# Kernel optimization log

Measured on AMD Instinct MI355X. Metric: run time of the kernel, lower is better.

The kernel has to match this reference:

```python
import jax, jax.numpy as jnp
import numpy as np

HIS = 10   # history steps (node_feature_dim = 10*4)
ROLL = 2   # args.pred_roll
MP = 2     # message_passing_steps
N = 20000  # num nodes (balls)
E = 320000 # num edges


def _mlp(x, W1, b1, W2, b2, g, be):
    # two-layer ELU MLP + BatchNorm1d (training mode: batch statistics)
    h = jax.nn.elu(x @ W1 + b1)
    h = jax.nn.elu(h @ W2 + b2)
    B, M, C = h.shape
    f = h.reshape(B * M, C)
    mu = f.mean(0)
    var = ((f - mu) ** 2).mean(0)  # biased variance, as torch BN training
    f = (f - mu) * jax.lax.rsqrt(var + 1e-5) * g + be
    return f.reshape(B, M, C)


def setup_inputs() -> dict:
    key = jax.random.key(0)
    ks = jax.random.split(key, 16)

    def lin(k, i, o):
        W = jax.random.normal(k, (i, o), jnp.float32) / jnp.sqrt(jnp.float32(i))
        b = jnp.full((o,), 0.1, jnp.float32)
        return W, b

    inp = {}
    inp["nodes"] = jax.random.normal(ks[0], (1, HIS + ROLL, N, 4), jnp.float32)
    inp["edge_pair"] = jax.random.randint(ks[1], (E, 2), 0, N)
    inp["edge_attr"] = jax.random.normal(ks[2], (E, 2), jnp.float32)
    # encoder node MLP: 40 -> 128 -> 128
    inp["en_W1"], inp["en_b1"] = lin(ks[3], 40, 128)
    inp["en_W2"], inp["en_b2"] = lin(ks[4], 128, 128)
    inp["en_g"], inp["en_be"] = jnp.ones((128,), jnp.float32), jnp.zeros((128,), jnp.float32)
    # encoder edge MLP: 6 -> 32 -> 32
    inp["ee_W1"], inp["ee_b1"] = lin(ks[5], 6, 32)
    inp["ee_W2"], inp["ee_b2"] = lin(ks[6], 32, 32)
    inp["ee_g"], inp["ee_be"] = jnp.ones((32,), jnp.float32), jnp.zeros((32,), jnp.float32)
    # GraphNetBlock edge MLP: 288 -> 128 -> 32
    inp["ge_W1"], inp["ge_b1"] = lin(ks[7], 288, 128)
    inp["ge_W2"], inp["ge_b2"] = lin(ks[8], 128, 32)
    inp["ge_g"], inp["ge_be"] = jnp.ones((32,), jnp.float32), jnp.zeros((32,), jnp.float32)
    # GraphNetBlock node MLP: 160 -> 256 -> 128
    inp["gn_W1"], inp["gn_b1"] = lin(ks[9], 160, 256)
    inp["gn_W2"], inp["gn_b2"] = lin(ks[10], 256, 128)
    inp["gn_g"], inp["gn_be"] = jnp.ones((128,), jnp.float32), jnp.zeros((128,), jnp.float32)
    # decoder: Linear(128,128) Tanh Linear(128,2)
    inp["d_W1"], inp["d_b1"] = lin(ks[11], 128, 128)
    inp["d_W2"], inp["d_b2"] = lin(ks[12], 128, 2)
    return inp


def _forward(nodes, edge_pair, edge_attr,
             en_W1, en_b1, en_W2, en_b2, en_g, en_be,
             ee_W1, ee_b1, ee_W2, ee_b2, ee_g, ee_be,
             ge_W1, ge_b1, ge_W2, ge_b2, ge_g, ge_be,
             gn_W1, gn_b1, gn_W2, gn_b2, gn_g, gn_be,
             d_W1, d_b1, d_W2, d_b2):
    window = nodes[0]                 # [T, N, 4]
    n = window.shape[1]
    s0 = edge_pair[:, 0]
    s1 = edge_pair[:, 1]
    # history features: [1, N, HIS*4]
    history = jnp.transpose(window[:HIS], (1, 0, 2)).reshape(1, n, -1)
    gt_future = window[HIS:]          # [ROLL, N, 4]
    # initial edge features: raw 2-dim attr + |pos/vel diff| (4-dim) -> 6
    pd0 = jnp.abs(window[HIS][s0] - window[HIS][s1])   # [E, 4]
    edge_feat = jnp.concatenate([edge_attr[None], pd0[None]], -1)  # [1, E, 6]
    cur_pos = window[HIS - 1, :, :2]
    cur_vel = window[HIS - 1, :, 2:]
    preds = []
    for _ in range(ROLL):
        ln = _mlp(history, en_W1, en_b1, en_W2, en_b2, en_g, en_be)    # [1,N,128]
        le = _mlp(edge_feat, ee_W1, ee_b1, ee_W2, ee_b2, ee_g, ee_be)  # [1,E,32]
        for _ in range(MP):
            # edge update: gather sender/receiver, MLP
            ef = jnp.concatenate([ln[:, s0], ln[:, s1], le], -1)       # [1,E,288]
            ne = _mlp(ef, ge_W1, ge_b1, ge_W2, ge_b2, ge_g, ge_be)     # [1,E,32]
            # node aggregation: scatter-add at both endpoints
            agg = jnp.zeros((n, ne.shape[-1]), ne.dtype)
            agg = agg.at[s0].add(ne[0]).at[s1].add(ne[0])
            nf = jnp.concatenate([ln, agg[None]], -1)                  # [1,N,160]
            nn_ = _mlp(nf, gn_W1, gn_b1, gn_W2, gn_b2, gn_g, gn_be)
            ln = nn_ + ln
            le = ne + le
        accel = jnp.tanh(ln @ d_W1 + d_b1) @ d_W2 + d_b2               # [1,N,2]
        prev_pos = cur_pos
        cur_pos = 2 * cur_pos + accel - prev_pos                       # [1,N,2]
        cur_vel = cur_vel + accel
        pd = jnp.abs(cur_pos[:, s0] - cur_pos[:, s1])                  # [1,E,2]
        edge_feat = edge_feat.at[:, :, -2:].set(pd)
        preds.append(cur_pos)
        hist4 = history.reshape(1, n, HIS, 4)
        new_state = jnp.concatenate([cur_pos.reshape(1, n, 1, 2),
                                     cur_vel.reshape(1, n, 1, 2)], -1)
        history = jnp.concatenate([hist4[:, :, 1:, :], new_state], -2).reshape(1, n, -1)
    preds = jnp.stack(preds, 1)                                        # [1,ROLL,N,2]
    diff = preds[0] - gt_future[:, :, :2]
    variance = 5e-5
    loss_nll = (diff ** 2 / (2 * variance)).sum() / (ROLL * n)
    loss_mse = (diff ** 2).mean()
    return preds, loss_nll, loss_mse, gt_future


def reference(nodes, edge_pair, edge_attr,
              en_W1, en_b1, en_W2, en_b2, en_g, en_be,
              ee_W1, ee_b1, ee_W2, ee_b2, ee_g, ee_be,
              ge_W1, ge_b1, ge_W2, ge_b2, ge_g, ge_be,
              gn_W1, gn_b1, gn_W2, gn_b2, gn_g, gn_be,
              d_W1, d_b1, d_W2, d_b2):
    return _forward(nodes, edge_pair, edge_attr,
                    en_W1, en_b1, en_W2, en_b2, en_g, en_be,
                    ee_W1, ee_b1, ee_W2, ee_b2, ee_g, ee_be,
                    ge_W1, ge_b1, ge_W2, ge_b2, ge_g, ge_be,
                    gn_W1, gn_b1, gn_W2, gn_b2, gn_g, gn_be,
                    d_W1, d_b1, d_W2, d_b2)
```

## Files before the change

kernel.cpp:

```cpp
#include <hip/hip_runtime.h>


constexpr int NN = 20000;
constexpr int NE = 320000;
constexpr int NSLOT = 32;
constexpr int SSTR = 512;

typedef __attribute__((ext_vector_type(8))) short short8;
typedef __attribute__((ext_vector_type(4))) float f32x4;

__device__ __forceinline__ float act_elu(float x) { return x > 0.f ? x : __expf(x) - 1.f; }
__device__ __forceinline__ unsigned short f2bf(float f) {
  unsigned u = __builtin_bit_cast(unsigned, f);
  return (unsigned short)((u + 0x7FFFu + ((u >> 16) & 1u)) >> 16);
}
__device__ __forceinline__ float bf2f(unsigned short h) {
  unsigned u = ((unsigned)h) << 16; return __builtin_bit_cast(float, u);
}

template<int K1, int K1P, int C1, int C2, int BM, int NWM, int NWC, int NWM2, int NWC2,
         int ACT2, bool STATS, int MODE>
__global__ __launch_bounds__(256) void mlp2_k(
    const unsigned short* __restrict__ A,
    const unsigned short* __restrict__ Wt1, const float* __restrict__ b1,
    const unsigned short* __restrict__ Wt2, const float* __restrict__ b2,
    unsigned short* __restrict__ out, int M, float* __restrict__ stat,
    float* __restrict__ aggF, const float* __restrict__ statP, float invE,
    const float* __restrict__ gg, const float* __restrict__ gb,
    float* __restrict__ sclW, const int* __restrict__ dg0, const int* __restrict__ dg1)
{
  constexpr int FM  = BM / (16 * NWM);
  constexpr int FC  = C1 / (16 * NWC);
  constexpr int FM2 = BM / (16 * NWM2);
  constexpr int FC2 = C2 / (16 * NWC2);
  constexpr int NKS1 = K1P / 32;
  constexpr int NKS2 = C1 / 32;
  constexpr int AST = K1P + 8;
  constexpr int P1 = C1 + 8;
  constexpr int P2 = C2 + 8;
  constexpr int ACH = K1P / 8;
  static_assert(NWM * NWC == 4 && NWM2 * NWC2 == 4, "4 waves");
  static_assert(C2 <= C1, "repack reuses H1");

  __shared__ unsigned short As[BM * AST];
  __shared__ unsigned short H1[BM * P1];
  __shared__ float red[2][C2];
  __shared__ float s_scl[(MODE == 4) ? 32 : 1], s_shf[(MODE == 4) ? 32 : 1];

  const int tid = threadIdx.x;
  const int row0 = blockIdx.x * BM;
  const int wave = tid >> 6, lane = tid & 63;
  const int wm = wave % NWM, wc = wave / NWM;
  const int wm2 = wave % NWM2, wc2 = wave / NWM2;
  const int lr = lane & 15, kg = lane >> 4;

  if (STATS) for (int i = tid; i < 2 * C2; i += 256) ((float*)red)[i] = 0.f;

  if constexpr (MODE == 4) {
    if (tid < 32) {
      float su = 0.f, sq = 0.f;
      for (int s = 0; s < NSLOT; ++s) {
        su += statP[(size_t)s * SSTR + tid];
        sq += statP[(size_t)s * SSTR + 256 + tid];
      }
      float mu = su * invE;
      float var = sq * invE - mu * mu;
      float sc = rsqrtf(var + 1e-5f) * gg[tid];
      float sh = gb[tid] - mu * sc;
      s_scl[tid] = sc; s_shf[tid] = sh;
      if (blockIdx.x == 0) { sclW[tid] = sc; sclW[32 + tid] = sh; }
    }
    __syncthreads();
  }

  for (int idx = tid; idx < BM * ACH; idx += 256) {
    int m = idx / ACH, chk = idx % ACH;
    int kglob = chk * 8;
    int row = row0 + m;
    uint4 v = make_uint4(0, 0, 0, 0);
    if (row < M) {
      if constexpr (MODE == 0) {
        if (kglob + 8 <= K1) v = *(const uint4*)(A + (size_t)row * K1 + kglob);
      } else if constexpr (MODE == 3) {
        if (chk == 0) v = *(const uint4*)(A + (size_t)row * 8);
      } else {
        if (kglob < 128) {
          v = *(const uint4*)(A + (size_t)row * 128 + kglob);
        } else {
          int c0 = kglob - 128;
          float* ap = &aggF[(size_t)row * 32 + c0];
          float4 a0 = *(float4*)ap, a1 = *(float4*)(ap + 4);
          *(float4*)ap = make_float4(0.f, 0.f, 0.f, 0.f);
          *(float4*)(ap + 4) = make_float4(0.f, 0.f, 0.f, 0.f);
          float d = (float)(dg0[row] + dg1[row]);
          float av[8] = {a0.x, a0.y, a0.z, a0.w, a1.x, a1.y, a1.z, a1.w};
          unsigned short* vp = (unsigned short*)&v;
#pragma unroll
          for (int j = 0; j < 8; ++j)
            vp[j] = f2bf(fmaf(s_scl[c0 + j], av[j], d * s_shf[c0 + j]));
        }
      }
    }
    *(uint4*)&As[m * AST + chk * 8] = v;
  }
  __syncthreads();

  f32x4 acc1[FM][FC];
#pragma unroll
  for (int i = 0; i < FM; ++i)
#pragma unroll
    for (int j = 0; j < FC; ++j) acc1[i][j] = (f32x4){0.f, 0.f, 0.f, 0.f};

#pragma unroll
  for (int ks = 0; ks < NKS1; ++ks) {
    const int k0 = ks * 32;
    short8 af[FM], bfr[FC];
#pragma unroll
    for (int i = 0; i < FM; ++i) {
      int r = (wm * FM + i) * 16 + lr;
      af[i] = __builtin_bit_cast(short8, *(const uint4*)&As[r * AST + k0 + kg * 8]);
    }
#pragma unroll
    for (int j = 0; j < FC; ++j) {
      int c = (wc * FC + j) * 16 + lr;
      bfr[j] = __builtin_bit_cast(short8, *(const uint4*)&Wt1[(size_t)c * K1P + k0 + kg * 8]);
    }
#pragma unroll
    for (int i = 0; i < FM; ++i)
#pragma unroll
      for (int j = 0; j < FC; ++j)
        acc1[i][j] = __builtin_amdgcn_mfma_f32_16x16x32_bf16(af[i], bfr[j], acc1[i][j], 0, 0, 0);
  }

  {
    float bl1[FC];
#pragma unroll
    for (int j = 0; j < FC; ++j) bl1[j] = b1[(wc * FC + j) * 16 + lr];
#pragma unroll
    for (int i = 0; i < FM; ++i)
#pragma unroll
      for (int t = 0; t < 4; ++t) {
        int rl = (wm * FM + i) * 16 + kg * 4 + t;
#pragma unroll
        for (int j = 0; j < FC; ++j)
          H1[rl * P1 + (wc * FC + j) * 16 + lr] = f2bf(act_elu(acc1[i][j][t] + bl1[j]));
      }
  }
  __syncthreads();

  f32x4 acc2[FM2][FC2];
#pragma unroll
  for (int i = 0; i < FM2; ++i)
#pragma unroll
    for (int j = 0; j < FC2; ++j) acc2[i][j] = (f32x4){0.f, 0.f, 0.f, 0.f};

#pragma unroll
  for (int ks = 0; ks < NKS2; ++ks) {
    const int k0 = ks * 32;
    short8 af[FM2], bfr[FC2];
#pragma unroll
    for (int i = 0; i < FM2; ++i) {
      int r = (wm2 * FM2 + i) * 16 + lr;
      af[i] = __builtin_bit_cast(short8, *(const uint4*)&H1[r * P1 + k0 + kg * 8]);
    }
#pragma unroll
    for (int j = 0; j < FC2; ++j) {
      int c = (wc2 * FC2 + j) * 16 + lr;
      bfr[j] = __builtin_bit_cast(short8, *(const uint4*)&Wt2[(size_t)c * C1 + k0 + kg * 8]);
    }
#pragma unroll
    for (int i = 0; i < FM2; ++i)
#pragma unroll
      for (int j = 0; j < FC2; ++j)
        acc2[i][j] = __builtin_amdgcn_mfma_f32_16x16x32_bf16(af[i], bfr[j], acc2[i][j], 0, 0, 0);
  }
  __syncthreads();

  float psum[FC2], psq[FC2], bl2[FC2];
#pragma unroll
  for (int j = 0; j < FC2; ++j) {
    psum[j] = 0.f; psq[j] = 0.f;
    bl2[j] = b2[(wc2 * FC2 + j) * 16 + lr];
  }
#pragma unroll
  for (int i = 0; i < FM2; ++i)
#pragma unroll
    for (int t = 0; t < 4; ++t) {
      int rl = (wm2 * FM2 + i) * 16 + kg * 4 + t;
      bool ok = (row0 + rl) < M;
#pragma unroll
      for (int j = 0; j < FC2; ++j) {
        float v = acc2[i][j][t] + bl2[j];
        if (ACT2 == 1) v = act_elu(v);
        else if (ACT2 == 2) v = tanhf(v);
        if (STATS && ok) { psum[j] += v; psq[j] += v * v; }
        H1[rl * P2 + (wc2 * FC2 + j) * 16 + lr] = f2bf(v);
      }
    }
  if (STATS) {
#pragma unroll
    for (int j = 0; j < FC2; ++j) {
      int c = (wc2 * FC2 + j) * 16 + lr;
      atomicAdd(&red[0][c], psum[j]);
      atomicAdd(&red[1][c], psq[j]);
    }
  }
  __syncthreads();
  for (int idx = tid; idx < BM * (C2 / 8); idx += 256) {
    int r = idx / (C2 / 8), cc = idx % (C2 / 8);
    int row = row0 + r;
    if (row < M)
      *(uint4*)&out[(size_t)row * C2 + cc * 8] = *(const uint4*)&H1[r * P2 + cc * 8];
  }
  if (STATS) {
    float* st = stat + (size_t)(blockIdx.x & (NSLOT - 1)) * SSTR;
    for (int i = tid; i < C2; i += 256) {
      atomicAdd(&st[i], red[0][i]);
      atomicAdd(&st[256 + i], red[1][i]);
    }
  }
}

template<int K, int C, int BM, int NWM, int NWC, int ACT, int DEC>
__global__ __launch_bounds__(256) void mgemm_k(
    const unsigned short* __restrict__ A,
    const unsigned short* __restrict__ Wt, const float* __restrict__ bias,
    unsigned short* __restrict__ out, int M,
    const float* __restrict__ W2f, const float* __restrict__ b2f,
    float* __restrict__ pos, float* __restrict__ vel, float* __restrict__ preds)
{
  constexpr int FM = BM / (16 * NWM);
  constexpr int FC = C / (16 * NWC);
  constexpr int NKS = K / 32;
  constexpr int AST = K + 8;
  constexpr int P2 = C + 8;
  constexpr int ACH = K / 8;
  static_assert(NWM * NWC == 4, "4 waves");

  __shared__ unsigned short As[BM * AST];
  __shared__ unsigned short Ob[BM * P2];
  __shared__ float Wl[DEC ? 256 : 1];

  const int tid = threadIdx.x;
  const int row0 = blockIdx.x * BM;
  const int wave = tid >> 6, lane = tid & 63;
  const int wm = wave % NWM, wc = wave / NWM;
  const int lr = lane & 15, kg = lane >> 4;

  for (int idx = tid; idx < BM * ACH; idx += 256) {
    int m = idx / ACH, chk = idx % ACH;
    int row = row0 + m;
    uint4 v = make_uint4(0, 0, 0, 0);
    if (row < M) v = *(const uint4*)(A + (size_t)row * K + chk * 8);
    *(uint4*)&As[m * AST + chk * 8] = v;
  }
  __syncthreads();

  f32x4 acc[FM][FC];
#pragma unroll
  for (int i = 0; i < FM; ++i)
#pragma unroll
    for (int j = 0; j < FC; ++j) acc[i][j] = (f32x4){0.f, 0.f, 0.f, 0.f};

#pragma unroll
  for (int ks = 0; ks < NKS; ++ks) {
    const int k0 = ks * 32;
    short8 af[FM], bfr[FC];
#pragma unroll
    for (int i = 0; i < FM; ++i) {
      int r = (wm * FM + i) * 16 + lr;
      af[i] = __builtin_bit_cast(short8, *(const uint4*)&As[r * AST + k0 + kg * 8]);
    }
#pragma unroll
    for (int j = 0; j < FC; ++j) {
      int c = (wc * FC + j) * 16 + lr;
      bfr[j] = __builtin_bit_cast(short8, *(const uint4*)&Wt[(size_t)c * K + k0 + kg * 8]);
    }
#pragma unroll
    for (int i = 0; i < FM; ++i)
#pragma unroll
      for (int j = 0; j < FC; ++j)
        acc[i][j] = __builtin_amdgcn_mfma_f32_16x16x32_bf16(af[i], bfr[j], acc[i][j], 0, 0, 0);
  }

  float bl[FC];
#pragma unroll
  for (int j = 0; j < FC; ++j) bl[j] = bias[(wc * FC + j) * 16 + lr];
#pragma unroll
  for (int i = 0; i < FM; ++i)
#pragma unroll
    for (int t = 0; t < 4; ++t) {
      int rl = (wm * FM + i) * 16 + kg * 4 + t;
#pragma unroll
      for (int j = 0; j < FC; ++j) {
        float v = acc[i][j][t] + bl[j];
        if (ACT == 1) v = act_elu(v);
        else if (ACT == 2) v = tanhf(v);
        Ob[rl * P2 + (wc * FC + j) * 16 + lr] = f2bf(v);
      }
    }
  if constexpr (DEC) Wl[tid] = W2f[tid];
  __syncthreads();
  if constexpr (DEC) {
    int rloc = tid >> 3, j = tid & 7;
    int row = row0 + rloc;
    float ax = 0.f, ay = 0.f;
#pragma unroll
    for (int kk = 0; kk < 16; ++kk) {
      int k = j + 8 * kk;
      float f = bf2f(Ob[rloc * P2 + k]);
      ax = fmaf(f, Wl[2 * k], ax);
      ay = fmaf(f, Wl[2 * k + 1], ay);
    }
    ax += __shfl_down(ax, 4, 8); ax += __shfl_down(ax, 2, 8); ax += __shfl_down(ax, 1, 8);
    ay += __shfl_down(ay, 4, 8); ay += __shfl_down(ay, 2, 8); ay += __shfl_down(ay, 1, 8);
    if (j == 0 && row < M) {
      float axx = ax + b2f[0], ayy = ay + b2f[1];
      float2 p = ((float2*)pos)[row], vv = ((float2*)vel)[row];
      p.x += axx; p.y += ayy; vv.x += axx; vv.y += ayy;
      ((float2*)pos)[row] = p; ((float2*)vel)[row] = vv;
      ((float2*)preds)[row] = p;
    }
  } else {
    for (int idx = tid; idx < BM * (C / 8); idx += 256) {
      int r = idx / (C / 8), cc = idx % (C / 8);
      int row = row0 + r;
      if (row < M)
        *(uint4*)&out[(size_t)row * C + cc * 8] = *(const uint4*)&Ob[r * P2 + cc * 8];
    }
  }
}

template<int WOUT, int LEFUSE>
__global__ __launch_bounds__(256) void ge_edge_k(
    const unsigned short* __restrict__ Pb,
    const unsigned short* __restrict__ leb,
    const unsigned short* __restrict__ e32prev,
    const float* __restrict__ sclshf,
    const int* __restrict__ epP,
    const unsigned short* __restrict__ Wt1c,
    const float* __restrict__ b1,
    const unsigned short* __restrict__ Wt2,
    const float* __restrict__ b2,
    unsigned short* __restrict__ out,
    float* __restrict__ aggF,
    float* __restrict__ stat)
{
  constexpr int BM = 64;
  constexpr int P1 = 136;
  __shared__ unsigned short Ps[BM * P1];
  __shared__ unsigned short As[BM * 40];
  __shared__ float red[2][32];
  __shared__ int eps[BM * 2];

  const int tid = threadIdx.x;
  const int e0 = blockIdx.x * BM;
  const int wave = tid >> 6, lane = tid & 63;
  const int lr = lane & 15, kg = lane >> 4;
  const int wm = wave & 1, wc = wave >> 1;

  uint4 g0[4], g1[4];
  int gm[4], gch[4];
#pragma unroll
  for (int t = 0; t < 4; ++t) {
    int idx = tid + 256 * t;
    int m = idx >> 4, ch = idx & 15;
    gm[t] = m; gch[t] = ch;
    int s0 = epP[2 * (e0 + m)];
    int s1 = epP[2 * (e0 + m) + 1];
    g0[t] = *(const uint4*)&Pb[(size_t)s0 * 256 + ch * 8];
    g1[t] = *(const uint4*)&Pb[(size_t)s1 * 256 + 128 + ch * 8];
  }

  if (tid < BM * 2) eps[tid] = epP[e0 * 2 + tid];
  {
    int m = tid >> 2, chk = tid & 3;
    uint4 lv = *(const uint4*)&leb[(size_t)(e0 + m) * 32 + chk * 8];
    if constexpr (LEFUSE) {
      uint4 ev = *(const uint4*)&e32prev[(size_t)(e0 + m) * 32 + chk * 8];
      const unsigned short* lp = (const unsigned short*)&lv;
      const unsigned short* epv = (const unsigned short*)&ev;
      uint4 ov;
      unsigned short* op = (unsigned short*)&ov;
#pragma unroll
      for (int j = 0; j < 8; ++j) {
        int c = chk * 8 + j;
        op[j] = f2bf(bf2f(lp[j]) + fmaf(sclshf[c], bf2f(epv[j]), sclshf[32 + c]));
      }
      *(uint4*)&As[m * 40 + chk * 8] = ov;
    } else {
      *(uint4*)&As[m * 40 + chk * 8] = lv;
    }
  }
  short8 wf1[4];
#pragma unroll
  for (int j = 0; j < 4; ++j)
    wf1[j] = __builtin_bit_cast(short8, *(const uint4*)&Wt1c[(size_t)((wc * 4 + j) * 16 + lr) * 32 + kg * 8]);
  if (tid < 64) ((float*)red)[tid] = 0.f;
  __syncthreads();

  f32x4 acc1[2][4];
#pragma unroll
  for (int i = 0; i < 2; ++i)
#pragma unroll
    for (int j = 0; j < 4; ++j) acc1[i][j] = (f32x4){0.f, 0.f, 0.f, 0.f};
  {
    short8 af[2];
#pragma unroll
    for (int i = 0; i < 2; ++i)
      af[i] = __builtin_bit_cast(short8, *(const uint4*)&As[((wm * 2 + i) * 16 + lr) * 40 + kg * 8]);
#pragma unroll
    for (int i = 0; i < 2; ++i)
#pragma unroll
      for (int j = 0; j < 4; ++j)
        acc1[i][j] = __builtin_amdgcn_mfma_f32_16x16x32_bf16(af[i], wf1[j], acc1[i][j], 0, 0, 0);
  }

#pragma unroll
  for (int t = 0; t < 4; ++t) {
    uint4 o;
    const unsigned short* ap = (const unsigned short*)&g0[t];
    const unsigned short* bp = (const unsigned short*)&g1[t];
    unsigned short* op = (unsigned short*)&o;
#pragma unroll
    for (int j = 0; j < 8; ++j) op[j] = f2bf(bf2f(ap[j]) + bf2f(bp[j]));
    *(uint4*)&Ps[gm[t] * P1 + gch[t] * 8] = o;
  }
  __syncthreads();

  {
    float bl1[4];
#pragma unroll
    for (int j = 0; j < 4; ++j) bl1[j] = b1[(wc * 4 + j) * 16 + lr];
#pragma unroll
    for (int i = 0; i < 2; ++i)
#pragma unroll
      for (int t = 0; t < 4; ++t) {
        int rl = (wm * 2 + i) * 16 + kg * 4 + t;
#pragma unroll
        for (int j = 0; j < 4; ++j) {
          int a = rl * P1 + (wc * 4 + j) * 16 + lr;
          Ps[a] = f2bf(act_elu(acc1[i][j][t] + bl1[j] + bf2f(Ps[a])));
        }
      }
  }
  __syncthreads();

  f32x4 acc2[2];
  acc2[0] = (f32x4){0.f, 0.f, 0.f, 0.f};
  acc2[1] = (f32x4){0.f, 0.f, 0.f, 0.f};
  const int r2 = wave * 16 + lr;
#pragma unroll
  for (int ks = 0; ks < 4; ++ks) {
    int k0 = ks * 32;
    short8 a2 = __builtin_bit_cast(short8, *(const uint4*)&Ps[r2 * P1 + k0 + kg * 8]);
#pragma unroll
    for (int j = 0; j < 2; ++j) {
      short8 b2f = __builtin_bit_cast(short8, *(const uint4*)&Wt2[(size_t)(j * 16 + lr) * 128 + k0 + kg * 8]);
      acc2[j] = __builtin_amdgcn_mfma_f32_16x16x32_bf16(a2, b2f, acc2[j], 0, 0, 0);
    }
  }

  float psum[2] = {0.f, 0.f}, psq[2] = {0.f, 0.f};
  float bl2[2] = {b2[lr], b2[16 + lr]};
#pragma unroll
  for (int t = 0; t < 4; ++t) {
    int rl = wave * 16 + kg * 4 + t;
#pragma unroll
    for (int j = 0; j < 2; ++j) {
      float v = act_elu(acc2[j][t] + bl2[j]);
      psum[j] += v; psq[j] += v * v;
      As[rl * 40 + j * 16 + lr] = f2bf(v);
    }
  }
#pragma unroll
  for (int j = 0; j < 2; ++j) {
    atomicAdd(&red[0][j * 16 + lr], psum[j]);
    atomicAdd(&red[1][j * 16 + lr], psq[j]);
  }
  __syncthreads();
  if (WOUT) {
    int m = tid >> 2, chk = tid & 3;
    *(uint4*)&out[(size_t)(e0 + m) * 32 + chk * 8] = *(const uint4*)&As[m * 40 + chk * 8];
  }
  {
    int c = tid & 31, gsel = tid >> 5;
    int rbeg = gsel * 8;
    float acc = 0.f;
    int cur = eps[2 * rbeg];
#pragma unroll
    for (int r = 0; r < 8; ++r) {
      int row = rbeg + r;
      float v = bf2f(As[row * 40 + c]);
      int s0 = eps[2 * row];
      if (s0 != cur) { atomicAdd(&aggF[(size_t)cur * 32 + c], acc); acc = 0.f; cur = s0; }
      acc += v;
      atomicAdd(&aggF[(size_t)eps[2 * row + 1] * 32 + c], v);
    }
    atomicAdd(&aggF[(size_t)cur * 32 + c], acc);
  }
  if (tid < 32) {
    float* st = stat + (size_t)(blockIdx.x & (NSLOT - 1)) * SSTR;
    atomicAdd(&st[tid], red[0][tid]);
    atomicAdd(&st[256 + tid], red[1][tid]);
  }
}

__global__ __launch_bounds__(256) void wtrans_all_k(
    const float* __restrict__ enW1, const float* __restrict__ enW2,
    const float* __restrict__ geW1, const float* __restrict__ geW2,
    const float* __restrict__ gnW1, const float* __restrict__ gnW2,
    const float* __restrict__ dW1,  const float* __restrict__ eeW1,
    const float* __restrict__ eeW2,
    unsigned short* __restrict__ enW1t, unsigned short* __restrict__ enW2t,
    unsigned short* __restrict__ gePt,  unsigned short* __restrict__ geCt,
    unsigned short* __restrict__ geW2t,
    unsigned short* __restrict__ gnW1t, unsigned short* __restrict__ gnW2t,
    unsigned short* __restrict__ dW1t,  unsigned short* __restrict__ eeW1t,
    unsigned short* __restrict__ eeW2t)
{
  int i = blockIdx.x * 256 + threadIdx.x;
#define SEG(Wsrc, Wdst, NROW, SRCS, KS, KP) \
  { int n = (NROW) * (KP); \
    if (i < n) { int c = i / (KP), k = i - c * (KP); \
      (Wdst)[i] = (k < (KS)) ? f2bf((Wsrc)[(size_t)k * (SRCS) + c]) : (unsigned short)0; return; } \
    i -= n; }
  SEG(enW1, enW1t, 128, 128, 40, 64)
  SEG(enW2, enW2t, 128, 128, 128, 128)
  SEG(geW1, gePt, 128, 128, 128, 128)
  SEG(geW1 + 128 * 128, gePt + 128 * 128, 128, 128, 128, 128)
  SEG(geW1 + 256 * 128, geCt, 128, 128, 32, 32)
  SEG(geW2, geW2t, 32, 32, 128, 128)
  SEG(gnW1, gnW1t, 256, 256, 160, 160)
  SEG(gnW2, gnW2t, 128, 128, 256, 256)
  SEG(dW1,  dW1t,  128, 128, 128, 128)
  SEG(eeW1, eeW1t, 32, 32, 6, 32)
  SEG(eeW2, eeW2t, 32, 32, 32, 32)
#undef SEG
}
constexpr int WT_TOTAL = 128*64 + 128*128 + 128*128 + 128*128 + 128*32 + 32*128
                       + 256*160 + 128*256 + 128*128 + 32*32 + 32*32;

template<int C, bool RES>
__global__ __launch_bounds__(256) void normb_k(const unsigned short* __restrict__ h,
    const float* __restrict__ stat, float invM,
    const float* __restrict__ g, const float* __restrict__ be,
    unsigned short* __restrict__ out_bf, int total8)
{
  __shared__ float s_scl[C], s_shf[C];
  for (int i = threadIdx.x; i < C; i += 256) {
    float su = 0.f, sq = 0.f;
    for (int s = 0; s < NSLOT; ++s) {
      su += stat[(size_t)s * SSTR + i];
      sq += stat[(size_t)s * SSTR + 256 + i];
    }
    float mu = su * invM;
    float var = sq * invM - mu * mu;
    float sc = rsqrtf(var + 1e-5f) * g[i];
    s_scl[i] = sc; s_shf[i] = be[i] - mu * sc;
  }
  __syncthreads();
  int i = blockIdx.x * 256 + threadIdx.x;
  if (i >= total8) return;
  int c8 = (i % (C / 8)) * 8;
  uint4 hv = ((const uint4*)h)[i];
  const unsigned short* hp = (const unsigned short*)&hv;
  float f[8];
#pragma unroll
  for (int j = 0; j < 8; ++j) f[j] = fmaf(bf2f(hp[j]), s_scl[c8 + j], s_shf[c8 + j]);
  if (RES) {
    uint4 pv = ((const uint4*)out_bf)[i];
    const unsigned short* pp = (const unsigned short*)&pv;
#pragma unroll
    for (int j = 0; j < 8; ++j) f[j] += bf2f(pp[j]);
  }
  uint4 o;
  unsigned short* op = (unsigned short*)&o;
#pragma unroll
  for (int j = 0; j < 8; ++j) op[j] = f2bf(f[j]);
  ((uint4*)out_bf)[i] = o;
}

__global__ __launch_bounds__(256) void csr_count0_k(const int* __restrict__ ep,
    int* __restrict__ deg0, int E)
{
  int e = blockIdx.x * 256 + threadIdx.x;
  if (e < E) atomicAdd(&deg0[ep[2 * e]], 1);
}

__global__ __launch_bounds__(1024) void csr_scan_k(const int* __restrict__ deg,
    int* __restrict__ off, int* __restrict__ cursor, int N)
{
  __shared__ int part[1024];
  int t = threadIdx.x;
  const int CHK = (N + 1023) / 1024;
  int c0 = t * CHK, c1 = min(c0 + CHK, N);
  int s = 0;
  for (int i = c0; i < c1; ++i) s += deg[i];
  part[t] = s;
  __syncthreads();
  for (int o = 1; o < 1024; o <<= 1) {
    int v = (t >= o) ? part[t - o] : 0;
    __syncthreads();
    part[t] += v;
    __syncthreads();
  }
  int run = t ? part[t - 1] : 0;
  for (int i = c0; i < c1; ++i) { int d = deg[i]; off[i] = run; cursor[i] = run; run += d; }
}

__global__ __launch_bounds__(256) void csr_fill0_k(const int* __restrict__ ep,
    int* __restrict__ cursor0, int* __restrict__ perm, int E)
{
  int e = blockIdx.x * 256 + threadIdx.x;
  if (e < E) { int p = atomicAdd(&cursor0[ep[2 * e]], 1); perm[p] = e; }
}

__global__ __launch_bounds__(256) void permute_edges_k(const float4* __restrict__ nodes4,
    const float* __restrict__ attr, const int* __restrict__ ep,
    const int* __restrict__ perm, int* __restrict__ epP,
    unsigned short* __restrict__ efb, int* __restrict__ deg1, int E)
{
  int e2 = blockIdx.x * 256 + threadIdx.x;
  if (e2 >= E) return;
  int e = perm[e2];
  int s0 = ep[2 * e], s1 = ep[2 * e + 1];
  epP[2 * e2] = s0; epP[2 * e2 + 1] = s1;
  atomicAdd(&deg1[s1], 1);
  float4 w0 = nodes4[(size_t)10 * NN + s0];
  float4 w1 = nodes4[(size_t)10 * NN + s1];
  float2 a = ((const float2*)attr)[e];
  uint4 o;
  o.x = (unsigned)f2bf(a.x) | ((unsigned)f2bf(a.y) << 16);
  o.y = (unsigned)f2bf(fabsf(w0.x - w1.x)) | ((unsigned)f2bf(fabsf(w0.y - w1.y)) << 16);
  o.z = (unsigned)f2bf(fabsf(w0.z - w1.z)) | ((unsigned)f2bf(fabsf(w0.w - w1.w)) << 16);
  o.w = 0;
  ((uint4*)efb)[e2] = o;
}

__global__ __launch_bounds__(256) void pd_upd_k(const float* __restrict__ pos,
    const int* __restrict__ epP, unsigned short* __restrict__ efb, int E)
{
  int e = blockIdx.x * 256 + threadIdx.x;
  if (e >= E) return;
  float2 p0 = ((const float2*)pos)[epP[2 * e]];
  float2 p1 = ((const float2*)pos)[epP[2 * e + 1]];
  unsigned u = (unsigned)f2bf(fabsf(p0.x - p1.x)) | ((unsigned)f2bf(fabsf(p0.y - p1.y)) << 16);
  *(unsigned*)&efb[(size_t)e * 8 + 4] = u;
}

__global__ __launch_bounds__(256) void hist_shift_k(float* __restrict__ hist,
    unsigned short* __restrict__ histb,
    const float* __restrict__ pos, const float* __restrict__ vel, int M)
{
  int n = blockIdx.x * 256 + threadIdx.x;
  if (n >= M) return;
  float4* h4 = (float4*)(hist + (size_t)n * 40);
  float4 tmp[10];
#pragma unroll
  for (int t = 0; t < 10; ++t) tmp[t] = h4[t];
  float2 pp = ((const float2*)pos)[n], vv = ((const float2*)vel)[n];
  unsigned* hb = (unsigned*)(histb + (size_t)n * 40);
#pragma unroll
  for (int t = 0; t < 9; ++t) {
    float4 v = tmp[t + 1];
    h4[t] = v;
    hb[2 * t]     = (unsigned)f2bf(v.x) | ((unsigned)f2bf(v.y) << 16);
    hb[2 * t + 1] = (unsigned)f2bf(v.z) | ((unsigned)f2bf(v.w) << 16);
  }
  float4 nv = make_float4(pp.x, pp.y, vv.x, vv.y);
  h4[9] = nv;
  hb[18] = (unsigned)f2bf(nv.x) | ((unsigned)f2bf(nv.y) << 16);
  hb[19] = (unsigned)f2bf(nv.z) | ((unsigned)f2bf(nv.w) << 16);
}

__global__ __launch_bounds__(256) void init_nodes_k(const float4* __restrict__ nodes4,
    float* __restrict__ hist, unsigned short* __restrict__ histb,
    float* __restrict__ pos, float* __restrict__ vel,
    float* __restrict__ outGt, int M)
{
  int n = blockIdx.x * 256 + threadIdx.x;
  if (n >= M) return;
  float4* h4 = (float4*)(hist + (size_t)n * 40);
  unsigned* hb = (unsigned*)(histb + (size_t)n * 40);
  float4 v;
#pragma unroll
  for (int t = 0; t < 10; ++t) {
    v = nodes4[(size_t)t * M + n];
    h4[t] = v;
    hb[2 * t]     = (unsigned)f2bf(v.x) | ((unsigned)f2bf(v.y) << 16);
    hb[2 * t + 1] = (unsigned)f2bf(v.z) | ((unsigned)f2bf(v.w) << 16);
  }
  ((float2*)pos)[n] = make_float2(v.x, v.y);
  ((float2*)vel)[n] = make_float2(v.z, v.w);
  float4 g0 = nodes4[(size_t)10 * M + n];
  float4 g1 = nodes4[(size_t)11 * M + n];
  float2* gt2 = (float2*)outGt;
  gt2[(size_t)2 * n + 0] = make_float2(g0.x, g0.y);
  gt2[(size_t)2 * n + 1] = make_float2(g0.z, g0.w);
  gt2[(size_t)2 * (M + n) + 0] = make_float2(g1.x, g1.y);
  gt2[(size_t)2 * (M + n) + 1] = make_float2(g1.z, g1.w);
}

__global__ __launch_bounds__(256) void loss_k(const float* __restrict__ preds,
    const float* __restrict__ gtf, float* __restrict__ acc)
{
  int i = blockIdx.x * 256 + threadIdx.x;
  float d2 = 0.f;
  if (i < 2 * NN * 2) {
    int r = i / (NN * 2);
    int rem = i - r * (NN * 2);
    int n = rem >> 1, c = rem & 1;
    float df = preds[i] - gtf[((size_t)r * NN + n) * 4 + c];
    d2 = df * df;
  }
#pragma unroll
  for (int o = 32; o > 0; o >>= 1) d2 += __shfl_down(d2, o, 64);
  __shared__ float sb[4];
  int lane = threadIdx.x & 63, w = threadIdx.x >> 6;
  if (lane == 0) sb[w] = d2;
  __syncthreads();
  if (threadIdx.x == 0) atomicAdd(acc, sb[0] + sb[1] + sb[2] + sb[3]);
}

__global__ void loss_write_k(const float* __restrict__ acc, float* __restrict__ o)
{
  float s = *acc;
  o[0] = s * 0.25f;
  o[1] = s * (1.f / 80000.f);
}

extern "C" void kernel_launch(void* const* d_in, const int* in_sizes, int n_in,
                              void* d_out, int out_size, void* d_ws, size_t ws_size,
                              hipStream_t stream)
{
  (void)in_sizes; (void)n_in; (void)out_size; (void)ws_size;
  const float* nodes = (const float*)d_in[0];
  const int*   ep    = (const int*)d_in[1];
  const float* eattr = (const float*)d_in[2];
  const float *en_W1 = (const float*)d_in[3],  *en_b1 = (const float*)d_in[4],
              *en_W2 = (const float*)d_in[5],  *en_b2 = (const float*)d_in[6],
              *en_g  = (const float*)d_in[7],  *en_be = (const float*)d_in[8];
  const float *ee_W1 = (const float*)d_in[9],  *ee_b1 = (const float*)d_in[10],
              *ee_W2 = (const float*)d_in[11], *ee_b2 = (const float*)d_in[12],
              *ee_g  = (const float*)d_in[13], *ee_be = (const float*)d_in[14];
  const float *ge_W1 = (const float*)d_in[15], *ge_b1 = (const float*)d_in[16],
              *ge_W2 = (const float*)d_in[17], *ge_b2 = (const float*)d_in[18],
              *ge_g  = (const float*)d_in[19], *ge_be = (const float*)d_in[20];
  const float *gn_W1 = (const float*)d_in[21], *gn_b1 = (const float*)d_in[22],
              *gn_W2 = (const float*)d_in[23], *gn_b2 = (const float*)d_in[24],
              *gn_g  = (const float*)d_in[25], *gn_be = (const float*)d_in[26];
  const float *d_W1  = (const float*)d_in[27], *d_b1  = (const float*)d_in[28],
              *d_W2  = (const float*)d_in[29], *d_b2  = (const float*)d_in[30];

  float* out = (float*)d_out;
  float* outPreds = out;
  float* outLoss  = out + 80000;
  float* outGt    = out + 80002;

  float* ws = (float*)d_ws;
  size_t off = 0;
  auto alloc = [&](size_t nf) { float* p = ws + off; off += (nf + 15) & ~(size_t)15; return p; };
  float* hist  = alloc((size_t)NN * 40);
  unsigned short* histb = (unsigned short*)alloc((size_t)NN * 20);
  unsigned short* efb   = (unsigned short*)alloc((size_t)NE * 4);
  unsigned short* lnb  = (unsigned short*)alloc((size_t)NN * 64);
  unsigned short* leb  = (unsigned short*)alloc((size_t)NE * 16);
  unsigned short* e32b = (unsigned short*)alloc((size_t)NE * 16);
  unsigned short* Pb   = (unsigned short*)alloc((size_t)NN * 128);
  unsigned short* h2nb = (unsigned short*)alloc((size_t)NN * 64);
  float* aggF  = alloc((size_t)NN * 32);
  float* pos   = alloc((size_t)NN * 2);
  float* vel   = alloc((size_t)NN * 2);
  unsigned short* enW1t = (unsigned short*)alloc(128 * 64 / 2);
  unsigned short* enW2t = (unsigned short*)alloc(128 * 128 / 2);
  unsigned short* gePt  = (unsigned short*)alloc(256 * 128 / 2);
  unsigned short* geCt  = (unsigned short*)alloc(128 * 32 / 2);
  unsigned short* geW2t = (unsigned short*)alloc(32 * 128 / 2);
  unsigned short* gnW1t = (unsigned short*)alloc(256 * 160 / 2);
  unsigned short* gnW2t = (unsigned short*)alloc(128 * 256 / 2);
  unsigned short* dW1t  = (unsigned short*)alloc(128 * 128 / 2);
  unsigned short* eeW1t = (unsigned short*)alloc(32 * 32 / 2);
  unsigned short* eeW2t = (unsigned short*)alloc(32 * 32 / 2);
  const size_t SLOTSZ = (size_t)NSLOT * SSTR;
  float* statArr = alloc(12 * SLOTSZ + 256 + 16);
  float* zerosF  = statArr + 12 * SLOTSZ;
  float* lacc    = zerosF + 256;
  float* sclshfGE = alloc(64);
  int* deg0    = (int*)alloc(NN);
  int* off0    = (int*)alloc(NN);
  int* cursor0 = (int*)alloc(NN);
  int* deg1    = (int*)alloc(NN);
  int* perm    = (int*)alloc(NE);
  int* epP     = (int*)alloc(2 * (size_t)NE);

  hipMemsetAsync(statArr, 0, (12 * SLOTSZ + 256 + 16) * sizeof(float), stream);
  hipMemsetAsync(deg0, 0, NN * sizeof(int), stream);
  hipMemsetAsync(deg1, 0, NN * sizeof(int), stream);
  hipMemsetAsync(aggF, 0, (size_t)NN * 32 * sizeof(float), stream);

  wtrans_all_k<<<(WT_TOTAL + 255) / 256, 256, 0, stream>>>(
      en_W1, en_W2, ge_W1, ge_W2, gn_W1, gn_W2, d_W1, ee_W1, ee_W2,
      enW1t, enW2t, gePt, geCt, geW2t, gnW1t, gnW2t, dW1t, eeW1t, eeW2t);

  init_nodes_k<<<(NN + 255) / 256, 256, 0, stream>>>((const float4*)nodes, hist, histb, pos, vel, outGt, NN);

  csr_count0_k<<<(NE + 255) / 256, 256, 0, stream>>>(ep, deg0, NE);
  csr_scan_k<<<1, 1024, 0, stream>>>(deg0, off0, cursor0, NN);
  csr_fill0_k<<<(NE + 255) / 256, 256, 0, stream>>>(ep, cursor0, perm, NE);
  permute_edges_k<<<(NE + 255) / 256, 256, 0, stream>>>(
      (const float4*)nodes, eattr, ep, perm, epP, efb, deg1, NE);

  const int GN32 = (NN + 31) / 32;
  const int GE128 = NE / 128;
  const int GE64 = NE / 64;
  const int G_N8 = (NN * 16 + 255) / 256;
  const int G_E8 = (NE * 4 + 255) / 256;
  const float invE = 1.f / NE;

  for (int r = 0; r < 2; ++r) {
    float* sEN = statArr + (size_t)(r * 6 + 0) * SLOTSZ;
    float* sEE = statArr + (size_t)(r * 6 + 1) * SLOTSZ;

    mlp2_k<40, 64, 128, 128, 32, 2, 2, 2, 2, 1, true, 0><<<GN32, 256, 0, stream>>>(
        histb, enW1t, en_b1, enW2t, en_b2, h2nb, NN, sEN,
        nullptr, nullptr, 0.f, nullptr, nullptr, nullptr, nullptr, nullptr);
    normb_k<128, false><<<G_N8, 256, 0, stream>>>(h2nb, sEN, 1.f / NN, en_g, en_be, lnb, NN * 16);

    mlp2_k<32, 32, 32, 32, 128, 4, 1, 4, 1, 1, true, 3><<<GE128, 256, 0, stream>>>(
        efb, eeW1t, ee_b1, eeW2t, ee_b2, e32b, NE, sEE,
        nullptr, nullptr, 0.f, nullptr, nullptr, nullptr, nullptr, nullptr);
    normb_k<32, false><<<G_E8, 256, 0, stream>>>(e32b, sEE, invE, ee_g, ee_be, leb, NE * 4);

    for (int mp = 0; mp < 2; ++mp) {
      float* sGE = statArr + (size_t)(r * 6 + 2 + mp * 2) * SLOTSZ;
      float* sGN = statArr + (size_t)(r * 6 + 3 + mp * 2) * SLOTSZ;

      mgemm_k<128, 256, 32, 2, 2, 0, 0><<<GN32, 256, 0, stream>>>(
          lnb, gePt, zerosF, Pb, NN, nullptr, nullptr, nullptr, nullptr, nullptr);
      if (mp == 0)
        ge_edge_k<1, 0><<<GE64, 256, 0, stream>>>(Pb, leb, nullptr, nullptr, epP,
            geCt, ge_b1, geW2t, ge_b2, e32b, aggF, sGE);
      else
        ge_edge_k<0, 1><<<GE64, 256, 0, stream>>>(Pb, leb, e32b, sclshfGE, epP,
            geCt, ge_b1, geW2t, ge_b2, nullptr, aggF, sGE);

      mlp2_k<160, 160, 256, 128, 32, 2, 2, 2, 2, 1, true, 4><<<GN32, 256, 0, stream>>>(
          lnb, gnW1t, gn_b1, gnW2t, gn_b2, h2nb, NN, sGN,
          aggF, sGE, invE, ge_g, ge_be, sclshfGE, deg0, deg1);
      normb_k<128, true><<<G_N8, 256, 0, stream>>>(h2nb, sGN, 1.f / NN, gn_g, gn_be, lnb, NN * 16);
    }

    mgemm_k<128, 128, 32, 2, 2, 2, 1><<<GN32, 256, 0, stream>>>(
        lnb, dW1t, d_b1, nullptr, NN, d_W2, d_b2, pos, vel, outPreds + (size_t)r * NN * 2);

    if (r == 0) {
      pd_upd_k<<<(NE + 255) / 256, 256, 0, stream>>>(pos, epP, efb, NE);
      hist_shift_k<<<(NN + 255) / 256, 256, 0, stream>>>(hist, histb, pos, vel, NN);
    }
  }

  loss_k<<<(2 * NN * 2 + 255) / 256, 256, 0, stream>>>(outPreds, outGt, lacc);
  loss_write_k<<<1, 1, 0, stream>>>(lacc, outLoss);
}
```

Before: 760.1 us.

## Fold BatchNorm apply into consumer GEMM and edge kernels, drop normb passes

Removes the standalone normb kernels. Node BatchNorm (plus the residual add) is now applied while staging the A tile inside mgemm_k, which also writes the normalized activations back for later residual use. Edge-encoder BatchNorm is applied on the fly inside ge_edge_k from precomputed scale and shift, instead of materializing a normalized edge tensor. The goal is to cut kernel launches and whole passes over the node and edge activation buffers. In exchange, every block recomputes the 32-slot stat reduction, and block 0 of one launch computes the edge scale and shift that the following kernel reads.

```diff
diff --git a/kernel.cpp b/kernel.cpp
--- a/kernel.cpp
+++ b/kernel.cpp
@@ -221,11 +221,16 @@
   }
 }
 
-template<int K, int C, int BM, int NWM, int NWC, int ACT, int DEC>
+template<int K, int C, int BM, int NWM, int NWC, int ACT, int DEC, int BNST>
 __global__ __launch_bounds__(256) void mgemm_k(
-    const unsigned short* __restrict__ A,
+    const unsigned short* __restrict__ Ah2,
+    unsigned short* __restrict__ Aln,
     const unsigned short* __restrict__ Wt, const float* __restrict__ bias,
     unsigned short* __restrict__ out, int M,
+    const float* __restrict__ statP, float invN,
+    const float* __restrict__ gv, const float* __restrict__ bev,
+    const float* __restrict__ pubStat, const float* __restrict__ pubG,
+    const float* __restrict__ pubBe, float invPub, float* __restrict__ pubW,
     const float* __restrict__ W2f, const float* __restrict__ b2f,
     float* __restrict__ pos, float* __restrict__ vel, float* __restrict__ preds)
 {
@@ -236,10 +241,12 @@
   constexpr int P2 = C + 8;
   constexpr int ACH = K / 8;
   static_assert(NWM * NWC == 4, "4 waves");
+  static_assert(BNST == 0 || K == 128, "BN staging assumes K=128");
 
   __shared__ unsigned short As[BM * AST];
   __shared__ unsigned short Ob[BM * P2];
   __shared__ float Wl[DEC ? 256 : 1];
+  __shared__ float s_scl[BNST ? 128 : 1], s_shf[BNST ? 128 : 1];
 
   const int tid = threadIdx.x;
   const int row0 = blockIdx.x * BM;
@@ -247,11 +254,63 @@
   const int wm = wave % NWM, wc = wave / NWM;
   const int lr = lane & 15, kg = lane >> 4;
 
+  if constexpr (BNST > 0) {
+    if (tid < 128) {
+      float su = 0.f, sq = 0.f;
+      for (int s = 0; s < NSLOT; ++s) {
+        su += statP[(size_t)s * SSTR + tid];
+        sq += statP[(size_t)s * SSTR + 256 + tid];
+      }
+      float mu = su * invN;
+      float var = sq * invN - mu * mu;
+      float sc = rsqrtf(var + 1e-5f) * gv[tid];
+      s_scl[tid] = sc; s_shf[tid] = bev[tid] - mu * sc;
+    }
+    if constexpr (BNST == 1) {
+      if (blockIdx.x == 0 && tid >= 128 && tid < 160) {
+        int c = tid - 128;
+        float su = 0.f, sq = 0.f;
+        for (int s = 0; s < NSLOT; ++s) {
+          su += pubStat[(size_t)s * SSTR + c];
+          sq += pubStat[(size_t)s * SSTR + 256 + c];
+        }
+        float mu = su * invPub;
+        float var = sq * invPub - mu * mu;
+        float sc = rsqrtf(var + 1e-5f) * pubG[c];
+        pubW[c] = sc; pubW[32 + c] = pubBe[c] - mu * sc;
+      }
+    }
+    __syncthreads();
+  }
+
   for (int idx = tid; idx < BM * ACH; idx += 256) {
     int m = idx / ACH, chk = idx % ACH;
+    int kglob = chk * 8;
     int row = row0 + m;
     uint4 v = make_uint4(0, 0, 0, 0);
-    if (row < M) v = *(const uint4*)(A + (size_t)row * K + chk * 8);
+    if (row < M) {
+      if constexpr (BNST == 0) {
+        v = *(const uint4*)(Ah2 + (size_t)row * K + kglob);
+      } else {
+        uint4 h = *(const uint4*)(Ah2 + (size_t)row * 128 + kglob);
+        const unsigned short* hp = (const unsigned short*)&h;
+        float f[8];
+#pragma unroll
+        for (int j = 0; j < 8; ++j)
+          f[j] = fmaf(bf2f(hp[j]), s_scl[kglob + j], s_shf[kglob + j]);
+        if constexpr (BNST >= 2) {
+          uint4 l = *(const uint4*)(Aln + (size_t)row * 128 + kglob);
+          const unsigned short* lp = (const unsigned short*)&l;
+#pragma unroll
+          for (int j = 0; j < 8; ++j) f[j] += bf2f(lp[j]);
+        }
+        unsigned short* vp = (unsigned short*)&v;
+#pragma unroll
+        for (int j = 0; j < 8; ++j) vp[j] = f2bf(f[j]);
+        if constexpr (BNST <= 2)
+          *(uint4*)(Aln + (size_t)row * 128 + kglob) = v;
+      }
+    }
     *(uint4*)&As[m * AST + chk * 8] = v;
   }
   __syncthreads();
@@ -331,12 +390,13 @@
   }
 }
 
-template<int WOUT, int LEFUSE>
+template<int LE, int WOUT>
 __global__ __launch_bounds__(256) void ge_edge_k(
     const unsigned short* __restrict__ Pb,
-    const unsigned short* __restrict__ leb,
-    const unsigned short* __restrict__ e32prev,
-    const float* __restrict__ sclshf,
+    const unsigned short* __restrict__ e32ee,
+    const unsigned short* __restrict__ e32ge,
+    const float* __restrict__ sclEE,
+    const float* __restrict__ sclGE,
     const int* __restrict__ epP,
     const unsigned short* __restrict__ Wt1c,
     const float* __restrict__ b1,
@@ -375,22 +435,29 @@
   if (tid < BM * 2) eps[tid] = epP[e0 * 2 + tid];
   {
     int m = tid >> 2, chk = tid & 3;
-    uint4 lv = *(const uint4*)&leb[(size_t)(e0 + m) * 32 + chk * 8];
-    if constexpr (LEFUSE) {
-      uint4 ev = *(const uint4*)&e32prev[(size_t)(e0 + m) * 32 + chk * 8];
-      const unsigned short* lp = (const unsigned short*)&lv;
-      const unsigned short* epv = (const unsigned short*)&ev;
-      uint4 ov;
-      unsigned short* op = (unsigned short*)&ov;
+    size_t base = (size_t)(e0 + m) * 32 + chk * 8;
+    uint4 ev = *(const uint4*)&e32ee[base];
+    const unsigned short* epv = (const unsigned short*)&ev;
+    uint4 ov;
+    unsigned short* op = (unsigned short*)&ov;
+    if constexpr (LE == 2) {
+      uint4 gv2 = *(const uint4*)&e32ge[base];
+      const unsigned short* gp = (const unsigned short*)&gv2;
 #pragma unroll
       for (int j = 0; j < 8; ++j) {
         int c = chk * 8 + j;
-        op[j] = f2bf(bf2f(lp[j]) + fmaf(sclshf[c], bf2f(epv[j]), sclshf[32 + c]));
-      }
-      *(uint4*)&As[m * 40 + chk * 8] = ov;
+        float le = fmaf(sclEE[c], bf2f(epv[j]), sclEE[32 + c])
+                 + fmaf(sclGE[c], bf2f(gp[j]), sclGE[32 + c]);
+        op[j] = f2bf(le);
+      }
     } else {
-      *(uint4*)&As[m * 40 + chk * 8] = lv;
-    }
+#pragma unroll
+      for (int j = 0; j < 8; ++j) {
+        int c = chk * 8 + j;
+        op[j] = f2bf(fmaf(sclEE[c], bf2f(epv[j]), sclEE[32 + c]));
+      }
+    }
+    *(uint4*)&As[m * 40 + chk * 8] = ov;
   }
   short8 wf1[4];
 #pragma unroll
@@ -456,8 +523,8 @@
     short8 a2 = __builtin_bit_cast(short8, *(const uint4*)&Ps[r2 * P1 + k0 + kg * 8]);
 #pragma unroll
     for (int j = 0; j < 2; ++j) {
-      short8 b2f = __builtin_bit_cast(short8, *(const uint4*)&Wt2[(size_t)(j * 16 + lr) * 128 + k0 + kg * 8]);
-      acc2[j] = __builtin_amdgcn_mfma_f32_16x16x32_bf16(a2, b2f, acc2[j], 0, 0, 0);
+      short8 b2v = __builtin_bit_cast(short8, *(const uint4*)&Wt2[(size_t)(j * 16 + lr) * 128 + k0 + kg * 8]);
+      acc2[j] = __builtin_amdgcn_mfma_f32_16x16x32_bf16(a2, b2v, acc2[j], 0, 0, 0);
     }
   }
 
@@ -541,46 +608,6 @@
 constexpr int WT_TOTAL = 128*64 + 128*128 + 128*128 + 128*128 + 128*32 + 32*128
                        + 256*160 + 128*256 + 128*128 + 32*32 + 32*32;
 
-template<int C, bool RES>
-__global__ __launch_bounds__(256) void normb_k(const unsigned short* __restrict__ h,
-    const float* __restrict__ stat, float invM,
-    const float* __restrict__ g, const float* __restrict__ be,
-    unsigned short* __restrict__ out_bf, int total8)
-{
-  __shared__ float s_scl[C], s_shf[C];
-  for (int i = threadIdx.x; i < C; i += 256) {
-    float su = 0.f, sq = 0.f;
-    for (int s = 0; s < NSLOT; ++s) {
-      su += stat[(size_t)s * SSTR + i];
-      sq += stat[(size_t)s * SSTR + 256 + i];
-    }
-    float mu = su * invM;
-    float var = sq * invM - mu * mu;
-    float sc = rsqrtf(var + 1e-5f) * g[i];
-    s_scl[i] = sc; s_shf[i] = be[i] - mu * sc;
-  }
-  __syncthreads();
-  int i = blockIdx.x * 256 + threadIdx.x;
-  if (i >= total8) return;
-  int c8 = (i % (C / 8)) * 8;
-  uint4 hv = ((const uint4*)h)[i];
-  const unsigned short* hp = (const unsigned short*)&hv;
-  float f[8];
-#pragma unroll
-  for (int j = 0; j < 8; ++j) f[j] = fmaf(bf2f(hp[j]), s_scl[c8 + j], s_shf[c8 + j]);
-  if (RES) {
-    uint4 pv = ((const uint4*)out_bf)[i];
-    const unsigned short* pp = (const unsigned short*)&pv;
-#pragma unroll
-    for (int j = 0; j < 8; ++j) f[j] += bf2f(pp[j]);
-  }
-  uint4 o;
-  unsigned short* op = (unsigned short*)&o;
-#pragma unroll
-  for (int j = 0; j < 8; ++j) op[j] = f2bf(f[j]);
-  ((uint4*)out_bf)[i] = o;
-}
-
 __global__ __launch_bounds__(256) void csr_count0_k(const int* __restrict__ ep,
     int* __restrict__ deg0, int E)
 {
@@ -765,8 +792,8 @@
   unsigned short* histb = (unsigned short*)alloc((size_t)NN * 20);
   unsigned short* efb   = (unsigned short*)alloc((size_t)NE * 4);
   unsigned short* lnb  = (unsigned short*)alloc((size_t)NN * 64);
-  unsigned short* leb  = (unsigned short*)alloc((size_t)NE * 16);
-  unsigned short* e32b = (unsigned short*)alloc((size_t)NE * 16);
+  unsigned short* e32ee = (unsigned short*)alloc((size_t)NE * 16);
+  unsigned short* e32ge = (unsigned short*)alloc((size_t)NE * 16);
   unsigned short* Pb   = (unsigned short*)alloc((size_t)NN * 128);
   unsigned short* h2nb = (unsigned short*)alloc((size_t)NN * 64);
   float* aggF  = alloc((size_t)NN * 32);
@@ -786,6 +813,7 @@
   float* statArr = alloc(12 * SLOTSZ + 256 + 16);
   float* zerosF  = statArr + 12 * SLOTSZ;
   float* lacc    = zerosF + 256;
+  float* sclshfEE = alloc(64);
   float* sclshfGE = alloc(64);
   int* deg0    = (int*)alloc(NN);
   int* off0    = (int*)alloc(NN);
@@ -814,45 +842,51 @@
   const int GN32 = (NN + 31) / 32;
   const int GE128 = NE / 128;
   const int GE64 = NE / 64;
-  const int G_N8 = (NN * 16 + 255) / 256;
-  const int G_E8 = (NE * 4 + 255) / 256;
   const float invE = 1.f / NE;
+  const float invN = 1.f / NN;
 
   for (int r = 0; r < 2; ++r) {
-    float* sEN = statArr + (size_t)(r * 6 + 0) * SLOTSZ;
-    float* sEE = statArr + (size_t)(r * 6 + 1) * SLOTSZ;
+    float* sEN  = statArr + (size_t)(r * 6 + 0) * SLOTSZ;
+    float* sEE  = statArr + (size_t)(r * 6 + 1) * SLOTSZ;
+    float* sGE0 = statArr + (size_t)(r * 6 + 2) * SLOTSZ;
+    float* sGN0 = statArr + (size_t)(r * 6 + 3) * SLOTSZ;
+    float* sGE1 = statArr + (size_t)(r * 6 + 4) * SLOTSZ;
+    float* sGN1 = statArr + (size_t)(r * 6 + 5) * SLOTSZ;
 
     mlp2_k<40, 64, 128, 128, 32, 2, 2, 2, 2, 1, true, 0><<<GN32, 256, 0, stream>>>(
         histb, enW1t, en_b1, enW2t, en_b2, h2nb, NN, sEN,
         nullptr, nullptr, 0.f, nullptr, nullptr, nullptr, nullptr, nullptr);
-    normb_k<128, false><<<G_N8, 256, 0, stream>>>(h2nb, sEN, 1.f / NN, en_g, en_be, lnb, NN * 16);
-
     mlp2_k<32, 32, 32, 32, 128, 4, 1, 4, 1, 1, true, 3><<<GE128, 256, 0, stream>>>(
-        efb, eeW1t, ee_b1, eeW2t, ee_b2, e32b, NE, sEE,
+        efb, eeW1t, ee_b1, eeW2t, ee_b2, e32ee, NE, sEE,
         nullptr, nullptr, 0.f, nullptr, nullptr, nullptr, nullptr, nullptr);
-    normb_k<32, false><<<G_E8, 256, 0, stream>>>(e32b, sEE, invE, ee_g, ee_be, leb, NE * 4);
-
-    for (int mp = 0; mp < 2; ++mp) {
-      float* sGE = statArr + (size_t)(r * 6 + 2 + mp * 2) * SLOTSZ;
-      float* sGN = statArr + (size_t)(r * 6 + 3 + mp * 2) * SLOTSZ;
-
-      mgemm_k<128, 256, 32, 2, 2, 0, 0><<<GN32, 256, 0, stream>>>(
-          lnb, gePt, zerosF, Pb, NN, nullptr, nullptr, nullptr, nullptr, nullptr);
-      if (mp == 0)
-        ge_edge_k<1, 0><<<GE64, 256, 0, stream>>>(Pb, leb, nullptr, nullptr, epP,
-            geCt, ge_b1, geW2t, ge_b2, e32b, aggF, sGE);
-      else
-        ge_edge_k<0, 1><<<GE64, 256, 0, stream>>>(Pb, leb, e32b, sclshfGE, epP,
-            geCt, ge_b1, geW2t, ge_b2, nullptr, aggF, sGE);
-
-      mlp2_k<160, 160, 256, 128, 32, 2, 2, 2, 2, 1, true, 4><<<GN32, 256, 0, stream>>>(
-          lnb, gnW1t, gn_b1, gnW2t, gn_b2, h2nb, NN, sGN,
-          aggF, sGE, invE, ge_g, ge_be, sclshfGE, deg0, deg1);
-      normb_k<128, true><<<G_N8, 256, 0, stream>>>(h2nb, sGN, 1.f / NN, gn_g, gn_be, lnb, NN * 16);
-    }
-
-    mgemm_k<128, 128, 32, 2, 2, 2, 1><<<GN32, 256, 0, stream>>>(
-        lnb, dW1t, d_b1, nullptr, NN, d_W2, d_b2, pos, vel, outPreds + (size_t)r * NN * 2);
+
+    mgemm_k<128, 256, 32, 2, 2, 0, 0, 1><<<GN32, 256, 0, stream>>>(
+        h2nb, lnb, gePt, zerosF, Pb, NN,
+        sEN, invN, en_g, en_be,
+        sEE, ee_g, ee_be, invE, sclshfEE,
+        nullptr, nullptr, nullptr, nullptr, nullptr);
+    ge_edge_k<1, 1><<<GE64, 256, 0, stream>>>(Pb, e32ee, nullptr, sclshfEE, nullptr,
+        epP, geCt, ge_b1, geW2t, ge_b2, e32ge, aggF, sGE0);
+    mlp2_k<160, 160, 256, 128, 32, 2, 2, 2, 2, 1, true, 4><<<GN32, 256, 0, stream>>>(
+        lnb, gnW1t, gn_b1, gnW2t, gn_b2, h2nb, NN, sGN0,
+        aggF, sGE0, invE, ge_g, ge_be, sclshfGE, deg0, deg1);
+
+    mgemm_k<128, 256, 32, 2, 2, 0, 0, 2><<<GN32, 256, 0, stream>>>(
+        h2nb, lnb, gePt, zerosF, Pb, NN,
+        sGN0, invN, gn_g, gn_be,
+        nullptr, nullptr, nullptr, 0.f, nullptr,
+        nullptr, nullptr, nullptr, nullptr, nullptr);
+    ge_edge_k<2, 0><<<GE64, 256, 0, stream>>>(Pb, e32ee, e32ge, sclshfEE, sclshfGE,
+        epP, geCt, ge_b1, geW2t, ge_b2, nullptr, aggF, sGE1);
+    mlp2_k<160, 160, 256, 128, 32, 2, 2, 2, 2, 1, true, 4><<<GN32, 256, 0, stream>>>(
+        lnb, gnW1t, gn_b1, gnW2t, gn_b2, h2nb, NN, sGN1,
+        aggF, sGE1, invE, ge_g, ge_be, sclshfGE, deg0, deg1);
+
+    mgemm_k<128, 128, 32, 2, 2, 2, 1, 3><<<GN32, 256, 0, stream>>>(
+        h2nb, lnb, dW1t, d_b1, nullptr, NN,
+        sGN1, invN, gn_g, gn_be,
+        nullptr, nullptr, nullptr, 0.f, nullptr,
+        d_W2, d_b2, pos, vel, outPreds + (size_t)r * NN * 2);
 
     if (r == 0) {
       pd_upd_k<<<(NE + 255) / 256, 256, 0, stream>>>(pos, epP, efb, NE);
```

Measured after the change: 722.4 us. 1.05x faster.
